# Kernel optimization log

Hardware: AMD Instinct MI355X
Metric: run time of the kernel (lower is better)

## Reference

```python
import jax, jax.numpy as jnp
import numpy as np

VOCAB = 100000; D = 300; F_NUM = 768
M = 64; N = 16
SURF_L = 4; CTX_L = 50; DOC_L = 100; BODY_L = 200
HEADS = 5


def _conv_relu_avg(x, W, b):
    # x: [B, L, D] tokens-embedded; conv1d (valid) + relu + global avgpool -> [B, F]
    y = jax.lax.conv_general_dilated(x.transpose(0, 2, 1), W, (1,), 'VALID',
                                     dimension_numbers=('NCH', 'OIH', 'NCH'))
    return jax.nn.relu(y + b[None, :, None]).mean(axis=2)


def _mha(q, k, v, num_heads=HEADS):
    # split-head scaled dot-product attention (no learned projections), q:[Lq,D] k,v:[Lk,D]
    Lq, Dm = q.shape
    hd = Dm // num_heads
    qh = q.reshape(Lq, num_heads, hd).transpose(1, 0, 2)
    kh = k.reshape(k.shape[0], num_heads, hd).transpose(1, 0, 2)
    vh = v.reshape(v.shape[0], num_heads, hd).transpose(1, 0, 2)
    att = jax.nn.softmax(jnp.einsum('hqd,hkd->hqk', qh, kh) * (1.0 / np.sqrt(hd)), axis=-1)
    out = jnp.einsum('hqk,hkd->hqd', att, vh)
    return out.transpose(1, 0, 2).reshape(Lq, Dm)


def _cos(a, b, eps=1e-6):
    na = jnp.maximum(jnp.sqrt((a * a).sum(-1)), eps)
    nb = jnp.maximum(jnp.sqrt((b * b).sum(-1)), eps)
    return (a * b).sum(-1) / (na * nb)


def setup_inputs() -> dict:
    key = jax.random.key(0)
    ks = jax.random.split(key, 20)
    inp = {}
    inp['mention_entity'] = jnp.ones((M, N), dtype=jnp.int32)
    inp['m'] = M
    inp['n'] = N
    inp['mention_vec'] = jax.random.randint(ks[0], (M, SURF_L), 0, VOCAB)
    inp['context_vec'] = jax.random.randint(ks[1], (M, CTX_L), 0, VOCAB)
    inp['doc_vec'] = jax.random.randint(ks[2], (DOC_L,), 0, VOCAB)
    inp['title_vec'] = jax.random.normal(ks[3], (N, F_NUM), dtype=jnp.float32)
    inp['body_vec'] = jax.random.randint(ks[4], (N, BODY_L), 0, VOCAB)
    inp['sfeats'] = jnp.zeros((N, 1), dtype=jnp.float32)
    inp['m2c_prior'] = jax.random.uniform(ks[5], (N,), dtype=jnp.float32)
    inp['men2cands'] = jax.random.randint(ks[6], (M, N), 0, VOCAB)
    inp['contexts_ids'] = jax.random.randint(ks[7], (M, CTX_L), 0, VOCAB)
    inp['hand_features'] = jax.random.uniform(ks[8], (N, 1), dtype=jnp.float32)
    inp['bert_doc_vec'] = jax.random.normal(ks[9], (1, F_NUM), dtype=jnp.float32)
    # learned parameters
    inp['embed_table'] = jax.random.normal(ks[10], (VOCAB, D), dtype=jnp.float32) * 0.1
    inp['conv_ms_w'] = jax.random.normal(ks[11], (F_NUM, D, 2), dtype=jnp.float32) * 0.05
    inp['conv_ms_b'] = jnp.zeros((F_NUM,), dtype=jnp.float32)
    inp['conv_mc_w'] = jax.random.normal(ks[12], (F_NUM, D, 5), dtype=jnp.float32) * 0.05
    inp['conv_mc_b'] = jnp.zeros((F_NUM,), dtype=jnp.float32)
    inp['layer_local_w'] = jax.random.normal(ks[13], (7,), dtype=jnp.float32) * 0.3
    inp['layer_local_b'] = jnp.zeros((), dtype=jnp.float32)
    inp['att_w1'] = jax.random.normal(ks[14], (600, 300), dtype=jnp.float32) * 0.05
    inp['att_b1'] = jnp.zeros((300,), dtype=jnp.float32)
    inp['att_w2'] = jax.random.normal(ks[15], (300, 1), dtype=jnp.float32) * 0.05
    inp['att_b2'] = jnp.zeros((), dtype=jnp.float32)
    return inp


def reference(mention_entity, m, n, mention_vec, context_vec, doc_vec, title_vec,
              body_vec, sfeats, m2c_prior, men2cands, contexts_ids, hand_features,
              bert_doc_vec, embed_table, conv_ms_w, conv_ms_b, conv_mc_w, conv_mc_b,
              layer_local_w, layer_local_b, att_w1, att_b1, att_w2, att_b2):
    # per-mention conv features (vectorized over all mentions at once)
    ms = _conv_relu_avg(embed_table[mention_vec], conv_ms_w, conv_ms_b)   # [M,768]
    mc = _conv_relu_avg(embed_table[context_vec], conv_mc_w, conv_mc_b)   # [M,768]
    md = bert_doc_vec[0]                                                  # [768]
    doc_emb = embed_table[doc_vec]                                        # [100,300]
    body_emb = embed_table[body_vec]                                      # [N,200,300]

    # per-candidate cross attention doc<->body, max-pooled over query positions
    att_d_b = jax.vmap(lambda b: _mha(doc_emb, b, b).max(axis=0))(body_emb)          # [N,300]
    att_b_d = jax.vmap(lambda b: _mha(b, doc_emb, doc_emb).max(axis=0))(body_emb)    # [N,300]
    comb = jnp.concatenate([att_d_b, att_b_d], axis=-1)                              # [N,600]
    att_score = jax.nn.sigmoid(jax.nn.relu(comb @ att_w1 + att_b1) @ att_w2 + att_b2)[:, 0]  # [N]

    # LocalCtxAttRanker: candidate-vs-context attention score
    ctx_emb = embed_table[contexts_ids]                                   # [M,50,300]
    cand_emb = embed_table[men2cands]                                     # [M,N,300]
    tok = jnp.einsum('mnd,mtd->mnt', cand_emb, ctx_emb)                   # [M,N,50]
    p = jax.nn.softmax(tok.max(axis=1), axis=-1)                          # [M,50]
    ctxv = jnp.einsum('mt,mtd->md', p, ctx_emb)                           # [M,300]
    local_att = jnp.einsum('mnd,md->mn', cand_emb, ctxv)                  # [M,N]

    cos_st = _cos(ms[:, None, :], title_vec[None, :, :])                  # [M,N]
    cos_dt = _cos(md[None, :], title_vec)                                 # [N]
    cos_ct = _cos(mc[:, None, :], title_vec[None, :, :])                  # [M,N]

    Mm = ms.shape[0]
    bc = lambda v: jnp.broadcast_to(v[None, :], (Mm, v.shape[0]))
    # feature order matches torch.cat((hand_fea, prior, localAtt, attScore, C_score))
    feats = jnp.stack([bc(hand_features[:, 0]), bc(m2c_prior), local_att,
                       bc(att_score), cos_st, bc(cos_dt), cos_ct], axis=-1)  # [M,N,7]
    score = feats @ layer_local_w + layer_local_b                         # [M,N]

    # per-mention standardization (unbiased std, as torch.std), softmax and uniform renorm
    mu = score.mean(axis=1, keepdims=True)
    sd = score.std(axis=1, keepdims=True, ddof=1)
    z = (score - mu) / sd
    sm = jax.nn.softmax(z, axis=1)
    zmin = z.min(axis=1, keepdims=True)
    zmax = z.max(axis=1, keepdims=True)
    u = (z + 1.0 - zmin) / (zmax - zmin)
    u = u / u.sum(axis=1, keepdims=True)
    return (z, sm, u)
```

## Files before the change

kernel.cpp:

```cpp
#include <hip/hip_runtime.h>

#define MM 64
#define NN 16
#define DDIM 300
#define FNUM 768
#define SURF_LL 4
#define CTX_LL 50
#define DOC_LL 100
#define BODY_LL 200
#define NHEADS 5
#define HDIM 60

#define GM 2944
#define GK 1536
#define GN 768

typedef unsigned short u16;
typedef unsigned int u32;
typedef __attribute__((ext_vector_type(8))) short short8;
typedef __attribute__((ext_vector_type(4))) float f32x4;

#define OFF_MSG    0
#define OFF_CTX2G  76800
#define OFF_CANDG  1036800
#define OFF_MS     1344000
#define OFF_MC     1393152
#define OFF_PV0    1442304
#define OFF_PV1    1461504
#define OFF_ASC    1495104
#define OFF_LATT   1495120
#define OFF_ABF    1496144
#define OFF_WTMC   (OFF_ABF + GM*GK/2)
#define OFF_WTMS   (OFF_WTMC + GN*GK/2)

__device__ __forceinline__ u16 f2bf(float x) {
  union { float f; u32 u; } v; v.f = x;
  u32 r = v.u + 0x7FFFu + ((v.u >> 16) & 1u);
  return (u16)(r >> 16);
}

__global__ __launch_bounds__(256) void mega_prep_kernel(
    const float* __restrict__ embed,
    const int* __restrict__ mention_vec,
    const int* __restrict__ context_vec,
    const int* __restrict__ contexts_ids,
    const int* __restrict__ men2cands,
    const float* __restrict__ Wmc,
    const float* __restrict__ Wms,
    float* __restrict__ dst, float* __restrict__ mc,
    float* __restrict__ att_logit,
    u32* __restrict__ Abf, u32* __restrict__ WTmc, float* __restrict__ WTms) {
  int bid = blockIdx.x;
  if (bid < 5250) {
    int e = bid * 256 + threadIdx.x;
    int row = e / DDIM;
    int col = e - row * DDIM;
    int tok;
    if (row < 256)       tok = mention_vec[row];
    else if (row < 3456) tok = contexts_ids[row - 256];
    else                 tok = men2cands[row - 3456];
    dst[e] = embed[(size_t)tok * DDIM + col];
  } else if (bid < 5442) {
    mc[(bid - 5250) * 256 + threadIdx.x] = 0.f;
  } else if (bid == 5442) {
    if (threadIdx.x < NN) att_logit[threadIdx.x] = 0.f;
  } else if (bid < 14275) {
    int idx = (bid - 5443) * 256 + threadIdx.x;
    int r = idx / (GK / 2);
    int kp = idx - r * (GK / 2);
    int k = kp * 2;
    int m = r / 46, t = r - m * 46;
    u32 out = 0;
#pragma unroll
    for (int j = 0; j < 2; j++) {
      int kj = k + j;
      u16 h = 0;
      if (kj < 1500) {
        int tap = kj / 300;
        int d = kj - tap * 300;
        int tok = context_vec[m * CTX_LL + t + tap];
        h = f2bf(embed[(size_t)tok * DDIM + d]);
      }
      out |= (u32)h << (16 * j);
    }
    Abf[idx] = out;
  } else if (bid < 16579) {
    int idx = (bid - 14275) * 256 + threadIdx.x;
    int n = idx / (GK / 2);
    int kp = idx - n * (GK / 2);
    int k = kp * 2;
    u32 out = 0;
#pragma unroll
    for (int j = 0; j < 2; j++) {
      int kj = k + j;
      u16 h = 0;
      if (kj < 1500) {
        int tap = kj / 300;
        int d = kj - tap * 300;
        h = f2bf(Wmc[(size_t)n * 1500 + d * 5 + tap]);
      }
      out |= (u32)h << (16 * j);
    }
    WTmc[idx] = out;
  } else {
    int idx = (bid - 16579) * 256 + threadIdx.x;
    int k = idx / FNUM;
    int f = idx - k * FNUM;
    WTms[idx] = Wms[(size_t)f * 600 + k];
  }
}

__device__ __forceinline__ void conv_gemm_body(
    const u16* __restrict__ A,
    const u16* __restrict__ B,
    const float* __restrict__ bias,
    float* __restrict__ mc, int g, float* __restrict__ smem) {
  int bn = g % (GN / 64), bm = g / (GN / 64);
  u16* As = (u16*)smem;
  u16* Bs = (u16*)(smem + 2304);
  int tid = threadIdx.x;
  int w = tid >> 6, lane = tid & 63;
  int wr = w >> 1, wc = w & 1;
  int lg = lane >> 4, lm = lane & 15;
  f32x4 acc[2][2];
#pragma unroll
  for (int i = 0; i < 2; i++)
#pragma unroll
    for (int j = 0; j < 2; j++) acc[i][j] = (f32x4)0.f;
  int c0row = tid >> 3, ck = (tid & 7) * 8;
  const u16* Ag = A + (size_t)(bm * 64) * GK;
  const u16* Bg = B + (size_t)(bn * 64) * GK;
  for (int kt = 0; kt < GK / 64; kt++) {
    int k0 = kt * 64;
    uint4 av0 = *(const uint4*)(Ag + (size_t)c0row * GK + k0 + ck);
    uint4 av1 = *(const uint4*)(Ag + (size_t)(c0row + 32) * GK + k0 + ck);
    uint4 bv0 = *(const uint4*)(Bg + (size_t)c0row * GK + k0 + ck);
    uint4 bv1 = *(const uint4*)(Bg + (size_t)(c0row + 32) * GK + k0 + ck);
    __syncthreads();
    *(uint4*)&As[c0row * 72 + ck] = av0;
    *(uint4*)&As[(c0row + 32) * 72 + ck] = av1;
    *(uint4*)&Bs[c0row * 72 + ck] = bv0;
    *(uint4*)&Bs[(c0row + 32) * 72 + ck] = bv1;
    __syncthreads();
#pragma unroll
    for (int kk = 0; kk < 2; kk++) {
      short8 af0 = *(const short8*)&As[(wr * 32 + lm) * 72 + kk * 32 + lg * 8];
      short8 af1 = *(const short8*)&As[(wr * 32 + 16 + lm) * 72 + kk * 32 + lg * 8];
      short8 bf0 = *(const short8*)&Bs[(wc * 32 + lm) * 72 + kk * 32 + lg * 8];
      short8 bf1 = *(const short8*)&Bs[(wc * 32 + 16 + lm) * 72 + kk * 32 + lg * 8];
      acc[0][0] = __builtin_amdgcn_mfma_f32_16x16x32_bf16(af0, bf0, acc[0][0], 0, 0, 0);
      acc[0][1] = __builtin_amdgcn_mfma_f32_16x16x32_bf16(af0, bf1, acc[0][1], 0, 0, 0);
      acc[1][0] = __builtin_amdgcn_mfma_f32_16x16x32_bf16(af1, bf0, acc[1][0], 0, 0, 0);
      acc[1][1] = __builtin_amdgcn_mfma_f32_16x16x32_bf16(af1, bf1, acc[1][1], 0, 0, 0);
    }
  }
#pragma unroll
  for (int mf = 0; mf < 2; mf++)
#pragma unroll
    for (int nf = 0; nf < 2; nf++) {
      int col = bn * 64 + wc * 32 + nf * 16 + lm;
      float bb = bias[col];
      int base = bm * 64 + wr * 32 + mf * 16 + lg * 4;
      int mcur = base / 46;
      float s = 0.f;
#pragma unroll
      for (int r = 0; r < 4; r++) {
        float v = fmaxf(acc[mf][nf][r] + bb, 0.f) * (1.0f / 46.0f);
        int mm = (base + r) / 46;
        if (mm != mcur) { atomicAdd(&mc[mcur * FNUM + col], s); s = 0.f; mcur = mm; }
        s += v;
      }
      atomicAdd(&mc[mcur * FNUM + col], s);
    }
}

__device__ __forceinline__ void conv_ms_body(
    const float* __restrict__ msg, const float* __restrict__ WT,
    const float* __restrict__ B, float* __restrict__ ms, int b) {
  int m = b / 3, fi = b - m * 3;
  int f = fi * 256 + threadIdx.x;
  const float* x = msg + m * SURF_LL * DDIM;
  float a0 = 0.f, a1 = 0.f, a2 = 0.f;
  for (int d = 0; d < DDIM; d++) {
    float v0 = x[d], v1 = x[DDIM + d], v2 = x[2 * DDIM + d], v3 = x[3 * DDIM + d];
    float wA = WT[(size_t)(2 * d) * FNUM + f];
    float wB = WT[(size_t)(2 * d + 1) * FNUM + f];
    a0 += v0 * wA + v1 * wB;
    a1 += v1 * wA + v2 * wB;
    a2 += v2 * wA + v3 * wB;
  }
  float bb = B[f];
  float r = fmaxf(a0 + bb, 0.f) + fmaxf(a1 + bb, 0.f) + fmaxf(a2 + bb, 0.f);
  ms[m * FNUM + f] = r * (1.0f / 3.0f);
}

template <int DIR>
__device__ __forceinline__ void scores_pv_body(
    const float* __restrict__ embed, const int* __restrict__ doc_vec,
    const int* __restrict__ body_vec, float* __restrict__ pvp, int b,
    float* __restrict__ smem) {
  constexpr int Lq = DIR ? 200 : 100;
  constexpr int Lk = DIR ? 100 : 200;
  constexpr int KPL = DIR ? 2 : 4;
  constexpr int NQT = DIR ? 7 : 4;
  constexpr int NHALF = DIR ? 1 : 2;
  int qt = b / 80;
  int rem = b - qt * 80;
  int n = rem / 5, h = rem - n * 5;
  const int* qids = DIR ? body_vec + n * BODY_LL : doc_vec;
  const int* kids = DIR ? doc_vec : body_vec + n * BODY_LL;
  float* Ks = smem;
  float* Qs = smem + 12400;
  float* Pl = smem + 12400;
  float* red = smem + 15600;
  for (int idx = threadIdx.x; idx < Lk * 15; idx += 256) {
    int r = idx / 15, c = idx - r * 15;
    float4 v = *(const float4*)(embed + (size_t)kids[r] * DDIM + h * HDIM + c * 4);
    float* dp = Ks + r * 62 + c * 4;
    dp[0] = v.x; dp[1] = v.y; dp[2] = v.z; dp[3] = v.w;
  }
  for (int idx = threadIdx.x; idx < 32 * 15; idx += 256) {
    int r = idx / 15, c = idx - r * 15;
    int q = qt * 32 + r; if (q >= Lq) q = Lq - 1;
    float4 v = *(const float4*)(embed + (size_t)qids[q] * DDIM + h * HDIM + c * 4);
    float* dp = Qs + r * 64 + c * 4;
    dp[0] = v.x; dp[1] = v.y; dp[2] = v.z; dp[3] = v.w;
  }
  __syncthreads();
  int w = threadIdx.x >> 6, lane = threadIdx.x & 63;
  int kcl[KPL];
#pragma unroll
  for (int j = 0; j < KPL; j++) {
    int kk = lane + 64 * j; kcl[j] = (kk < Lk) ? kk : (Lk - 1);
  }
  float acc[8][KPL];
#pragma unroll
  for (int i = 0; i < 8; i++)
#pragma unroll
    for (int j = 0; j < KPL; j++) acc[i][j] = 0.f;
  for (int d = 0; d < HDIM; d += 4) {
    float2 kva[KPL], kvb[KPL];
#pragma unroll
    for (int j = 0; j < KPL; j++) {
      kva[j] = *(const float2*)&Ks[kcl[j] * 62 + d];
      kvb[j] = *(const float2*)&Ks[kcl[j] * 62 + d + 2];
    }
#pragma unroll
    for (int i = 0; i < 8; i++) {
      float4 qv = *(const float4*)&Qs[(w * 8 + i) * 64 + d];
#pragma unroll
      for (int j = 0; j < KPL; j++)
        acc[i][j] += qv.x * kva[j].x + qv.y * kva[j].y +
                     qv.z * kvb[j].x + qv.w * kvb[j].y;
    }
  }
  const float scale = 0.12909944487358056f;
#pragma unroll
  for (int i = 0; i < 8; i++) {
    float mx = -1e30f;
#pragma unroll
    for (int j = 0; j < KPL; j++)
      if (lane + 64 * j < Lk) mx = fmaxf(mx, acc[i][j]);
#pragma unroll
    for (int o = 32; o >= 1; o >>= 1) mx = fmaxf(mx, __shfl_xor(mx, o));
    float mxs = mx * scale;
    float p[KPL];
    float s = 0.f;
#pragma unroll
    for (int j = 0; j < KPL; j++) {
      p[j] = (lane + 64 * j < Lk) ? __expf(acc[i][j] * scale - mxs) : 0.f;
      s += p[j];
    }
#pragma unroll
    for (int o = 32; o >= 1; o >>= 1) s += __shfl_xor(s, o);
    float inv = 1.0f / s;
#pragma unroll
    for (int j = 0; j < KPL; j++) acc[i][j] = p[j] * inv;
  }
  __syncthreads();
  float o[8];
#pragma unroll
  for (int i = 0; i < 8; i++) o[i] = 0.f;
  int dl = (lane < HDIM) ? lane : (HDIM - 1);
#pragma unroll
  for (int half = 0; half < NHALF; half++) {
    int kbase = half * 100;
#pragma unroll
    for (int j = 0; j < KPL; j++) {
      int kk = lane + 64 * j;
      int rel = kk - kbase;
      if (rel >= 0 && rel < 100 && kk < Lk) {
#pragma unroll
        for (int i = 0; i < 8; i++)
          Pl[(w * 8 + i) * 100 + rel] = acc[i][j];
      }
    }
    for (int k4 = 0; k4 < 25; k4++) {
      int k = kbase + k4 * 4;
      float kv0 = Ks[(k + 0) * 62 + dl];
      float kv1 = Ks[(k + 1) * 62 + dl];
      float kv2 = Ks[(k + 2) * 62 + dl];
      float kv3 = Ks[(k + 3) * 62 + dl];
#pragma unroll
      for (int i = 0; i < 8; i++) {
        float4 pq = *(const float4*)&Pl[(w * 8 + i) * 100 + k4 * 4];
        o[i] += pq.x * kv0 + pq.y * kv1 + pq.z * kv2 + pq.w * kv3;
      }
    }
  }
  float omax = -1e30f;
#pragma unroll
  for (int i = 0; i < 8; i++) {
    int q = qt * 32 + w * 8 + i;
    if (q < Lq) omax = fmaxf(omax, o[i]);
  }
  red[w * 64 + lane] = omax;
  __syncthreads();
  if (threadIdx.x < 64 && lane < HDIM) {
    float m4 = fmaxf(fmaxf(red[0 * 64 + lane], red[1 * 64 + lane]),
                     fmaxf(red[2 * 64 + lane], red[3 * 64 + lane]));
    pvp[((size_t)(n * NHEADS + h) * NQT + qt) * HDIM + lane] = m4;
  }
}

__device__ __forceinline__ void tokctxv_body(
    const float* __restrict__ candg, const float* __restrict__ ctx2g,
    float* __restrict__ local_att, int m, float* __restrict__ smem) {
  float* cand  = smem;
  float* ctx   = smem + 4800;
  float* tokb  = smem + 9600;
  float* tkmx  = smem + 9872;
  float* pp    = smem + 9936;
  float* sctxv = smem + 10000;
  int tid = threadIdx.x;
  for (int i = tid; i < NN * DDIM; i += 256)
    cand[i] = candg[(size_t)m * NN * DDIM + i];
  int nI = tid >> 4, tt = tid & 15;
  for (int tile = 0; tile < 4; tile++) {
    int cbase = tile * 16;
    __syncthreads();
    for (int i = tid; i < 16 * DDIM; i += 256) {
      int rr = i / DDIM, cc = i - rr * DDIM;
      int t = cbase + rr;
      ctx[rr * DDIM + cc] = (t < CTX_LL) ? ctx2g[(size_t)(m * CTX_LL + t) * DDIM + cc] : 0.f;
    }
    __syncthreads();
    const float4* ca = (const float4*)(cand + nI * DDIM);
    const float4* cb = (const float4*)(ctx + tt * DDIM);
    float dsum = 0.f;
#pragma unroll
    for (int c = 0; c < 75; c++) {
      float4 a = ca[c], b = cb[c];
      dsum += a.x * b.x + a.y * b.y + a.z * b.z + a.w * b.w;
    }
    tokb[nI * 17 + tt] = dsum;
    __syncthreads();
    if (tid < 16) {
      float mx = -1e30f;
      for (int nn = 0; nn < NN; nn++) mx = fmaxf(mx, tokb[nn * 17 + tid]);
      int t = cbase + tid;
      if (t < CTX_LL) tkmx[t] = mx;
    }
  }
  __syncthreads();
  if (tid < 64) {
    float v = (tid < CTX_LL) ? tkmx[tid] : -1e30f;
    float mx = v;
#pragma unroll
    for (int o = 32; o >= 1; o >>= 1) mx = fmaxf(mx, __shfl_xor(mx, o));
    float e = (tid < CTX_LL) ? expf(v - mx) : 0.f;
    float s = e;
#pragma unroll
    for (int o = 32; o >= 1; o >>= 1) s += __shfl_xor(s, o);
    pp[tid] = e / s;
  }
  __syncthreads();
  for (int d = tid; d < DDIM; d += 256) {
    float acc = 0.f;
    for (int t = 0; t < CTX_LL; t++)
      acc += pp[t] * ctx2g[(size_t)(m * CTX_LL + t) * DDIM + d];
    sctxv[d] = acc;
  }
  __syncthreads();
  int j = tid & 15;
  float dd = 0.f;
  for (int i = j; i < DDIM; i += 16) dd += cand[nI * DDIM + i] * sctxv[i];
#pragma unroll
  for (int o = 8; o >= 1; o >>= 1) dd += __shfl_xor(dd, o);
  if (j == 0) local_att[m * NN + nI] = dd;
}

__global__ __launch_bounds__(256) void mega_mid_kernel(
    const float* __restrict__ embed,
    const int* __restrict__ doc_vec,
    const int* __restrict__ body_vec,
    const float* __restrict__ msg,
    const float* __restrict__ WTms,
    const float* __restrict__ Bms,
    const float* __restrict__ candg,
    const float* __restrict__ ctx2g,
    const u16* __restrict__ Abf,
    const u16* __restrict__ WTmc,
    const float* __restrict__ Bmc,
    float* __restrict__ ms,
    float* __restrict__ mc,
    float* __restrict__ pv0,
    float* __restrict__ pv1,
    float* __restrict__ local_att) {
  __shared__ float smem[15856];
  int bid = blockIdx.x;
  if (bid < 192) {
    conv_ms_body(msg, WTms, Bms, ms, bid);
  } else if (bid < 512) {
    scores_pv_body<0>(embed, doc_vec, body_vec, pv0, bid - 192, smem);
  } else if (bid < 1072) {
    scores_pv_body<1>(embed, doc_vec, body_vec, pv1, bid - 512, smem);
  } else if (bid < 1136) {
    tokctxv_body(candg, ctx2g, local_att, bid - 1072, smem);
  } else {
    conv_gemm_body(Abf, WTmc, Bmc, mc, bid - 1136, smem);
  }
}

__global__ __launch_bounds__(256) void mlp_kernel(
    const float* __restrict__ pv0, const float* __restrict__ pv1,
    const float* __restrict__ w1, const float* __restrict__ b1,
    const float* __restrict__ w2,
    float* __restrict__ att_logit) {
  int bid = blockIdx.x;
  int n = bid / 5, jc = bid - n * 5;
  int tid = threadIdx.x;
  __shared__ float comb[600];
  __shared__ float partial[4][64];
  for (int idx = tid; idx < 600; idx += 256) {
    int side = idx >= 300;
    int pos = idx - side * 300;
    int h = pos / 60, d = pos - h * 60;
    float mx = -1e30f;
    if (!side) {
#pragma unroll
      for (int pt = 0; pt < 4; pt++)
        mx = fmaxf(mx, pv0[(size_t)((n * NHEADS + h) * 4 + pt) * HDIM + d]);
    } else {
#pragma unroll
      for (int pt = 0; pt < 7; pt++)
        mx = fmaxf(mx, pv1[(size_t)((n * NHEADS + h) * 7 + pt) * HDIM + d]);
    }
    comb[idx] = mx;
  }
  __syncthreads();
  int w = tid >> 6, lane = tid & 63;
  int jl = (lane < 60) ? lane : 59;
  int jg = jc * 60 + jl;
  float acc = 0.f;
  for (int k = w; k < 600; k += 4)
    acc += comb[k] * w1[(size_t)k * 300 + jg];
  partial[w][lane] = acc;
  __syncthreads();
  if (tid < 64) {
    float hv = partial[0][lane] + partial[1][lane] +
               partial[2][lane] + partial[3][lane];
    float hj = fmaxf(hv + b1[jg], 0.f) * w2[jg];
    if (lane >= 60) hj = 0.f;
#pragma unroll
    for (int o = 32; o >= 1; o >>= 1) hj += __shfl_xor(hj, o);
    if (lane == 0) atomicAdd(&att_logit[n], hj);
  }
}

__global__ __launch_bounds__(256) void final_kernel(
    const float* __restrict__ ms,
    const float* __restrict__ mc,
    const float* __restrict__ title,
    const float* __restrict__ bert,
    const float* __restrict__ att_logit,
    const float* __restrict__ b2,
    const float* __restrict__ m2c_prior,
    const float* __restrict__ hand,
    const float* __restrict__ local_att,
    const float* __restrict__ w7,
    const float* __restrict__ b7,
    float* __restrict__ out) {
  int m = blockIdx.x, tid = threadIdx.x;
  __shared__ float sms[FNUM], smc[FNUM], smd[FNUM];
  __shared__ float snorm[3], sscore[16], wred[3][4];
  for (int i = tid; i < FNUM; i += 256) {
    sms[i] = ms[m * FNUM + i];
    smc[i] = mc[m * FNUM + i];
    smd[i] = bert[i];
  }
  __syncthreads();
  float p1 = 0.f, p2 = 0.f, p3 = 0.f;
  for (int i = tid; i < FNUM; i += 256) {
    float a = sms[i], b = smc[i], c = smd[i];
    p1 += a * a; p2 += b * b; p3 += c * c;
  }
#pragma unroll
  for (int o = 32; o >= 1; o >>= 1) {
    p1 += __shfl_xor(p1, o); p2 += __shfl_xor(p2, o); p3 += __shfl_xor(p3, o);
  }
  int wid = tid >> 6, lane = tid & 63;
  if (lane == 0) { wred[0][wid] = p1; wred[1][wid] = p2; wred[2][wid] = p3; }
  __syncthreads();
  if (tid == 0) {
    snorm[0] = fmaxf(sqrtf(wred[0][0] + wred[0][1] + wred[0][2] + wred[0][3]), 1e-6f);
    snorm[1] = fmaxf(sqrtf(wred[1][0] + wred[1][1] + wred[1][2] + wred[1][3]), 1e-6f);
    snorm[2] = fmaxf(sqrtf(wred[2][0] + wred[2][1] + wred[2][2] + wred[2][3]), 1e-6f);
  }
  __syncthreads();
  int nI = tid >> 4, j = tid & 15;
  float d1 = 0.f, d2 = 0.f, d3 = 0.f, d4 = 0.f;
  for (int i = j; i < FNUM; i += 16) {
    float t = title[nI * FNUM + i];
    d1 += sms[i] * t; d2 += smc[i] * t; d3 += smd[i] * t; d4 += t * t;
  }
#pragma unroll
  for (int o = 8; o >= 1; o >>= 1) {
    d1 += __shfl_xor(d1, o); d2 += __shfl_xor(d2, o);
    d3 += __shfl_xor(d3, o); d4 += __shfl_xor(d4, o);
  }
  if (j == 0) {
    float nt = fmaxf(sqrtf(d4), 1e-6f);
    float cos_st = d1 / (snorm[0] * nt);
    float cos_ct = d2 / (snorm[1] * nt);
    float cos_dt = d3 / (snorm[2] * nt);
    float asc = 1.0f / (1.0f + expf(-(att_logit[nI] + b2[0])));
    float score = hand[nI] * w7[0] + m2c_prior[nI] * w7[1] +
                  local_att[m * NN + nI] * w7[2] + asc * w7[3] +
                  cos_st * w7[4] + cos_dt * w7[5] + cos_ct * w7[6] + b7[0];
    sscore[nI] = score;
  }
  __syncthreads();
  if (tid < 16) {
    float x = sscore[tid];
    float s = x;
#pragma unroll
    for (int o = 8; o >= 1; o >>= 1) s += __shfl_xor(s, o);
    float mu = s * (1.0f / 16.0f);
    float dv = (x - mu) * (x - mu);
    float vs = dv;
#pragma unroll
    for (int o = 8; o >= 1; o >>= 1) vs += __shfl_xor(vs, o);
    float sd = sqrtf(vs * (1.0f / 15.0f));
    float z = (x - mu) / sd;
    float zm = z;
#pragma unroll
    for (int o = 8; o >= 1; o >>= 1) zm = fmaxf(zm, __shfl_xor(zm, o));
    float e = expf(z - zm);
    float es = e;
#pragma unroll
    for (int o = 8; o >= 1; o >>= 1) es += __shfl_xor(es, o);
    float sm = e / es;
    float zmin = z;
#pragma unroll
    for (int o = 8; o >= 1; o >>= 1) zmin = fminf(zmin, __shfl_xor(zmin, o));
    float u0 = (z + 1.0f - zmin) / (zm - zmin);
    float us = u0;
#pragma unroll
    for (int o = 8; o >= 1; o >>= 1) us += __shfl_xor(us, o);
    float u = u0 / us;
    out[m * NN + tid] = z;
    out[MM * NN + m * NN + tid] = sm;
    out[2 * MM * NN + m * NN + tid] = u;
  }
}

extern "C" void kernel_launch(void* const* d_in, const int* in_sizes, int n_in,
                              void* d_out, int out_size, void* d_ws, size_t ws_size,
                              hipStream_t stream) {
  const int*   mention_vec   = (const int*)d_in[3];
  const int*   context_vec   = (const int*)d_in[4];
  const int*   doc_vec       = (const int*)d_in[5];
  const float* title_vec     = (const float*)d_in[6];
  const int*   body_vec      = (const int*)d_in[7];
  const float* m2c_prior     = (const float*)d_in[9];
  const int*   men2cands     = (const int*)d_in[10];
  const int*   contexts_ids  = (const int*)d_in[11];
  const float* hand_features = (const float*)d_in[12];
  const float* bert_doc_vec  = (const float*)d_in[13];
  const float* embed_table   = (const float*)d_in[14];
  const float* conv_ms_w     = (const float*)d_in[15];
  const float* conv_ms_b     = (const float*)d_in[16];
  const float* conv_mc_w     = (const float*)d_in[17];
  const float* conv_mc_b     = (const float*)d_in[18];
  const float* layer_local_w = (const float*)d_in[19];
  const float* layer_local_b = (const float*)d_in[20];
  const float* att_w1        = (const float*)d_in[21];
  const float* att_b1        = (const float*)d_in[22];
  const float* att_w2        = (const float*)d_in[23];
  const float* att_b2        = (const float*)d_in[24];

  float* ws     = (float*)d_ws;
  float* msg    = ws + OFF_MSG;
  float* ctx2g  = ws + OFF_CTX2G;
  float* candg  = ws + OFF_CANDG;
  float* ms     = ws + OFF_MS;
  float* mc     = ws + OFF_MC;
  float* pv0    = ws + OFF_PV0;
  float* pv1    = ws + OFF_PV1;
  float* att_lg = ws + OFF_ASC;
  float* latt   = ws + OFF_LATT;
  u16*   Abf    = (u16*)(ws + OFF_ABF);
  u16*   WTmc   = (u16*)(ws + OFF_WTMC);
  float* WTms   = ws + OFF_WTMS;
  float* out    = (float*)d_out;

  mega_prep_kernel<<<dim3(18379), dim3(256), 0, stream>>>(
      embed_table, mention_vec, context_vec, contexts_ids, men2cands,
      conv_mc_w, conv_ms_w, ws, mc, att_lg, (u32*)Abf, (u32*)WTmc, WTms);
  mega_mid_kernel<<<dim3(1688), dim3(256), 0, stream>>>(
      embed_table, doc_vec, body_vec, msg, WTms, conv_ms_b, candg, ctx2g,
      Abf, WTmc, conv_mc_b, ms, mc, pv0, pv1, latt);
  mlp_kernel<<<dim3(80), dim3(256), 0, stream>>>(
      pv0, pv1, att_w1, att_b1, att_w2, att_lg);
  final_kernel<<<dim3(MM), dim3(256), 0, stream>>>(
      ms, mc, title_vec, bert_doc_vec, att_lg, att_b2, m2c_prior,
      hand_features, latt, layer_local_w, layer_local_b, out);
}
```

Measured before the change: 375.8 us.

## Vectorize prep kernel gathers and use LDS tiles for weight transposes

```diff
diff --git a/kernel.cpp b/kernel.cpp
--- a/kernel.cpp
+++ b/kernel.cpp
@@ -39,6 +39,14 @@
   return (u16)(r >> 16);
 }
 
+#define PREP_GATHER_END  1313
+#define PREP_MCZ_END     1361
+#define PREP_LOGIT       1361
+#define PREP_ABUILD_BEG  1362
+#define PREP_ABUILD_END  3570
+#define PREP_WTMC_END    4338
+#define PREP_WTMS_END    4458
+
 __global__ __launch_bounds__(256) void mega_prep_kernel(
     const float* __restrict__ embed,
     const int* __restrict__ mention_vec,
@@ -50,63 +58,84 @@
     float* __restrict__ dst, float* __restrict__ mc,
     float* __restrict__ att_logit,
     u32* __restrict__ Abf, u32* __restrict__ WTmc, float* __restrict__ WTms) {
+  __shared__ float psm[4160];
   int bid = blockIdx.x;
-  if (bid < 5250) {
-    int e = bid * 256 + threadIdx.x;
-    int row = e / DDIM;
-    int col = e - row * DDIM;
-    int tok;
-    if (row < 256)       tok = mention_vec[row];
-    else if (row < 3456) tok = contexts_ids[row - 256];
-    else                 tok = men2cands[row - 3456];
-    dst[e] = embed[(size_t)tok * DDIM + col];
-  } else if (bid < 5442) {
-    mc[(bid - 5250) * 256 + threadIdx.x] = 0.f;
-  } else if (bid == 5442) {
-    if (threadIdx.x < NN) att_logit[threadIdx.x] = 0.f;
-  } else if (bid < 14275) {
-    int idx = (bid - 5443) * 256 + threadIdx.x;
-    int r = idx / (GK / 2);
-    int kp = idx - r * (GK / 2);
-    int k = kp * 2;
+  int tid = threadIdx.x;
+  if (bid < PREP_GATHER_END) {
+    int e4 = bid * 256 + tid;
+    if (e4 < 4480 * 75) {
+      int row = e4 / 75, c4 = e4 - row * 75;
+      int tok;
+      if (row < 256)       tok = mention_vec[row];
+      else if (row < 3456) tok = contexts_ids[row - 256];
+      else                 tok = men2cands[row - 3456];
+      float4 v = *(const float4*)(embed + (size_t)tok * DDIM + c4 * 4);
+      *(float4*)(dst + (size_t)row * DDIM + c4 * 4) = v;
+    }
+  } else if (bid < PREP_MCZ_END) {
+    int e4 = (bid - PREP_GATHER_END) * 256 + tid;
+    *(float4*)(mc + e4 * 4) = make_float4(0.f, 0.f, 0.f, 0.f);
+  } else if (bid == PREP_LOGIT) {
+    if (tid < NN) att_logit[tid] = 0.f;
+  } else if (bid < PREP_ABUILD_END) {
+    int idx4 = (bid - PREP_ABUILD_BEG) * 256 + tid;
+    int r = idx4 / (GK / 8);
+    int kq = idx4 - r * (GK / 8);
     int m = r / 46, t = r - m * 46;
-    u32 out = 0;
-#pragma unroll
-    for (int j = 0; j < 2; j++) {
-      int kj = k + j;
-      u16 h = 0;
-      if (kj < 1500) {
-        int tap = kj / 300;
-        int d = kj - tap * 300;
-        int tok = context_vec[m * CTX_LL + t + tap];
-        h = f2bf(embed[(size_t)tok * DDIM + d]);
+    int kbase = kq * 8;
+    u32 wlo[4];
+#pragma unroll
+    for (int q = 0; q < 4; q++) {
+      u32 outw = 0;
+#pragma unroll
+      for (int j = 0; j < 2; j++) {
+        int kj = kbase + q * 2 + j;
+        u16 h = 0;
+        if (kj < 1500) {
+          int tap = kj / 300;
+          int d = kj - tap * 300;
+          int tok = context_vec[m * CTX_LL + t + tap];
+          h = f2bf(embed[(size_t)tok * DDIM + d]);
+        }
+        outw |= (u32)h << (16 * j);
       }
-      out |= (u32)h << (16 * j);
-    }
-    Abf[idx] = out;
-  } else if (bid < 16579) {
-    int idx = (bid - 14275) * 256 + threadIdx.x;
-    int n = idx / (GK / 2);
-    int kp = idx - n * (GK / 2);
-    int k = kp * 2;
-    u32 out = 0;
-#pragma unroll
-    for (int j = 0; j < 2; j++) {
-      int kj = k + j;
-      u16 h = 0;
-      if (kj < 1500) {
-        int tap = kj / 300;
-        int d = kj - tap * 300;
-        h = f2bf(Wmc[(size_t)n * 1500 + d * 5 + tap]);
+      wlo[q] = outw;
+    }
+    ((uint4*)Abf)[idx4] = make_uint4(wlo[0], wlo[1], wlo[2], wlo[3]);
+  } else if (bid < PREP_WTMC_END) {
+    int n = bid - PREP_ABUILD_END;
+    for (int i = tid; i < 1500; i += 256) psm[i] = Wmc[(size_t)n * 1500 + i];
+    __syncthreads();
+    for (int kp = tid; kp < GK / 2; kp += 256) {
+      u32 outw = 0;
+#pragma unroll
+      for (int j = 0; j < 2; j++) {
+        int kj = kp * 2 + j;
+        u16 h = 0;
+        if (kj < 1500) {
+          int tap = kj / 300;
+          int d = kj - tap * 300;
+          h = f2bf(psm[d * 5 + tap]);
+        }
+        outw |= (u32)h << (16 * j);
       }
-      out |= (u32)h << (16 * j);
-    }
-    WTmc[idx] = out;
+      WTmc[(size_t)n * (GK / 2) + kp] = outw;
+    }
   } else {
-    int idx = (bid - 16579) * 256 + threadIdx.x;
-    int k = idx / FNUM;
-    int f = idx - k * FNUM;
-    WTms[idx] = Wms[(size_t)f * 600 + k];
+    int tile = bid - PREP_WTMC_END;
+    int kt = tile / 12, ft = tile - kt * 12;
+    int k0 = kt * 64, f0 = ft * 64;
+    for (int idx = tid; idx < 64 * 64; idx += 256) {
+      int i = idx >> 6, j = idx & 63;
+      if (k0 + j < 600)
+        psm[j * 65 + i] = Wms[(size_t)(f0 + i) * 600 + (k0 + j)];
+    }
+    __syncthreads();
+    for (int idx = tid; idx < 64 * 64; idx += 256) {
+      int j = idx >> 6, i = idx & 63;
+      if (k0 + j < 600)
+        WTms[(size_t)(k0 + j) * FNUM + (f0 + i)] = psm[j * 65 + i];
+    }
   }
 }
 
@@ -605,7 +634,7 @@
   float* WTms   = ws + OFF_WTMS;
   float* out    = (float*)d_out;
 
-  mega_prep_kernel<<<dim3(18379), dim3(256), 0, stream>>>(
+  mega_prep_kernel<<<dim3(PREP_WTMS_END), dim3(256), 0, stream>>>(
       embed_table, mention_vec, context_vec, contexts_ids, men2cands,
       conv_mc_w, conv_ms_w, ws, mc, att_lg, (u32*)Abf, (u32*)WTmc, WTms);
   mega_mid_kernel<<<dim3(1688), dim3(256), 0, stream>>>(
```

New measurement: 376.3 us (median of 2 runs). No clear change (+0.2%).
